# Kernel optimization log

Hardware: AMD Instinct MI355X
Metric: run time of the kernel (lower is better)

Reference implementation:

```python
import jax, jax.numpy as jnp
from jax import lax
import numpy as np

EPS_DENOM = 1e-5
EPS_NCC = 1e-5
HIGH = 0.5  # IntensityNormalization(high=0.5): min-max rescale of weights to [0, high]


def _box_conv(v, kernel):
    # Dense ones-kernel 3D box filter, VALID padding, stride 1 (NCDHW / OIDHW).
    return lax.conv_general_dilated(
        v, kernel, window_strides=(1, 1, 1), padding='VALID',
        dimension_numbers=('NCDHW', 'OIDHW', 'NCDHW'))


def setup_inputs() -> dict:
    key = jax.random.key(0)
    k1, k2 = jax.random.split(key)
    shape = (2, 1, 160, 192, 160)
    y_pred = jax.random.normal(k1, shape, dtype=jnp.float32)
    y_true = jax.random.normal(k2, shape, dtype=jnp.float32)
    kernel = jnp.ones((1, 1, 7, 7, 7), dtype=jnp.float32)
    return {"y_pred": y_pred, "y_true": y_true, "kernel": kernel}


def reference(y_pred, y_true, kernel):
    nw = kernel.sum()  # = 343 for a 7^3 ones kernel
    x, y = y_pred, y_true
    sum_x = _box_conv(x, kernel)
    sum_y = _box_conv(y, kernel)
    sum_x2 = _box_conv(x * x, kernel)
    sum_y2 = _box_conv(y * y, kernel)
    sum_xy = _box_conv(x * y, kernel)

    mean_x = sum_x / nw
    mean_y = sum_y / nw
    num = sum_xy + mean_x * mean_y * nw - mean_x * sum_y - mean_y * sum_x
    denom_0 = mean_x * mean_x * nw + sum_x2 - 2.0 * mean_x * sum_x
    denom_1 = mean_y * mean_y * nw + sum_y2 - 2.0 * mean_y * sum_y
    denom = denom_0 * denom_1

    valid = denom > EPS_DENOM
    safe_denom = jnp.where(valid, denom, 1.0)
    ncc = jnp.where(valid, num / jnp.sqrt(safe_denom), 0.0)
    invalid = (ncc < -1.0 - EPS_NCC) | (ncc > 1.0 + EPS_NCC)
    ncc = jnp.where(invalid, 0.0, ncc)
    all_valid = valid & ~invalid

    # Intensity normalization of weights: min-max rescale of local variance sum
    # over the valid voxels to [0, HIGH], then normalize to sum to 1.
    v = 0.5 * (denom_0 + denom_1)
    vmin = jnp.min(jnp.where(all_valid, v, jnp.inf))
    vmax = jnp.max(jnp.where(all_valid, v, -jnp.inf))
    w = jnp.where(all_valid, (v - vmin) / (vmax - vmin + 1e-12) * HIGH, 0.0)
    w = w / w.sum()

    return 1.0 - jnp.sum(jnp.where(all_valid, ncc, 0.0) * w)
```

## Files before the change

kernel.cpp:

```cpp
#include <hip/hip_runtime.h>
#include <math.h>

#define NN 2
#define DD 160
#define HH 192
#define WW 160
#define DO 154
#define HO 186
#define WO 154

#define NWO 3
#define HOT 8
#define NHO 24
#define ZCH 7
#define ZOC 22
#define NSL 28
#define NB (NWO * NHO * NN * ZCH)

#define LDS_SYNC() do { __builtin_amdgcn_s_waitcnt(0xC07F); __builtin_amdgcn_s_barrier(); } while (0)

__device__ __forceinline__ float block_sum(float v, float* sm) {
  int tid = threadIdx.x;
  sm[tid] = v;
  __syncthreads();
#pragma unroll
  for (int off = 128; off > 0; off >>= 1) {
    if (tid < off) sm[tid] += sm[tid + off];
    __syncthreads();
  }
  float r = sm[0];
  __syncthreads();
  return r;
}

__device__ __forceinline__ float block_min(float v, float* sm) {
  int tid = threadIdx.x;
  sm[tid] = v;
  __syncthreads();
#pragma unroll
  for (int off = 128; off > 0; off >>= 1) {
    if (tid < off) sm[tid] = fminf(sm[tid], sm[tid + off]);
    __syncthreads();
  }
  float r = sm[0];
  __syncthreads();
  return r;
}

__device__ __forceinline__ float wave_sum(float v) {
  v += __shfl_xor(v, 32); v += __shfl_xor(v, 16); v += __shfl_xor(v, 8);
  v += __shfl_xor(v, 4);  v += __shfl_xor(v, 2);  v += __shfl_xor(v, 1);
  return v;
}

__device__ __forceinline__ float wave_min(float v) {
  v = fminf(v, __shfl_xor(v, 32)); v = fminf(v, __shfl_xor(v, 16));
  v = fminf(v, __shfl_xor(v, 8));  v = fminf(v, __shfl_xor(v, 4));
  v = fminf(v, __shfl_xor(v, 2));  v = fminf(v, __shfl_xor(v, 1));
  return v;
}

#define SLIDE7(V, M) do { \
  float s0 = ((V[0]+V[1])+(V[2]+V[3])) + ((V[4]+V[5])+V[6]); \
  float s1 = s0 - V[0] + V[7]; \
  float s2 = s1 - V[1] + V[8]; \
  float s3 = s2 - V[2] + V[9]; \
  *(float4*)&R[M][rA][c4] = make_float4(s0, s1, s2, s3); \
} while (0)

__global__ __launch_bounds__(256, 3) void ncc_fused(const float* __restrict__ X,
                                                    const float* __restrict__ Y,
                                                    float* __restrict__ part) {
  __shared__ __align__(16) float R[5][14][64];
  __shared__ __align__(16) float Mh[5][HOT][64];
  __shared__ float red[4][5];

  const int tid = threadIdx.x;
  const int tx = tid & 63, ty = tid >> 6;
  const int wo0 = blockIdx.x * 64;
  const int ho0 = blockIdx.y * HOT;
  const int n   = blockIdx.z / ZCH;
  const int ck  = blockIdx.z % ZCH;
  const int z0  = ck * ZOC;

  const int wo = wo0 + tx;
  const bool act0 = (wo < WO) && (ho0 + ty < HO);
  const bool act1 = (wo < WO) && (ho0 + ty + 4 < HO);

  const size_t slice = (size_t)HH * WW;
  const float* Xn = X + (size_t)n * DD * slice;
  const float* Yn = Y + (size_t)n * DD * slice;
  const float inv_nw = 1.0f / 343.0f;
  const float LO = -1.0f - 1e-5f, HI = 1.0f + 1e-5f;

  const int pA  = tid;
  const bool hasA = (pA < 224);
  const int rA  = pA >> 4;
  const int c4  = (pA & 15) << 2;
  const int hA  = ho0 + rA;
  const int baseW = wo0 + c4;
  const bool okA  = hasA && (hA < HH) && (baseW < WO);
  const bool tail = okA && (baseW + 10 > WW);
  const float* XrowA = Xn + (size_t)hA * WW + baseW;
  const float* YrowA = Yn + (size_t)hA * WW + baseW;

  float4 lx0={0,0,0,0}, lx1={0,0,0,0};
  float4 ly0={0,0,0,0}, ly1={0,0,0,0};
  float2 lx2={0,0}, ly2={0,0};

  auto loadA = [&](int s_in) {
    if (okA) {
      const float* xp = XrowA + (size_t)(z0 + s_in) * slice;
      const float* yp = YrowA + (size_t)(z0 + s_in) * slice;
      lx0 = *(const float4*)xp;       lx1 = *(const float4*)(xp + 4);
      ly0 = *(const float4*)yp;       ly1 = *(const float4*)(yp + 4);
      if (!tail) { lx2 = *(const float2*)(xp + 8); ly2 = *(const float2*)(yp + 8); }
      else       { lx2 = make_float2(0.f, 0.f);    ly2 = make_float2(0.f, 0.f); }
    }
  };

  auto storeA = [&]() {
    if (okA) {
      const float x[10] = {lx0.x,lx0.y,lx0.z,lx0.w, lx1.x,lx1.y,lx1.z,lx1.w, lx2.x,lx2.y};
      const float y[10] = {ly0.x,ly0.y,ly0.z,ly0.w, ly1.x,ly1.y,ly1.z,ly1.w, ly2.x,ly2.y};
      SLIDE7(x, 0);
      SLIDE7(y, 1);
      {
        float t[10];
#pragma unroll
        for (int i = 0; i < 10; ++i) t[i] = x[i] * x[i];
        SLIDE7(t, 2);
      }
      {
        float t[10];
#pragma unroll
        for (int i = 0; i < 10; ++i) t[i] = y[i] * y[i];
        SLIDE7(t, 3);
      }
      {
        float t[10];
#pragma unroll
        for (int i = 0; i < 10; ++i) t[i] = x[i] * y[i];
        SLIDE7(t, 4);
      }
    }
  };

  auto phaseHitem = [&](int ch, int w) {
    const float* rp = &R[ch][0][w];
    float r0=rp[0],   r1=rp[64],  r2=rp[128], r3=rp[192], r4=rp[256],
          r5=rp[320], r6=rp[384], r7=rp[448], r8=rp[512], r9=rp[576],
          r10=rp[640], r11=rp[704], r12=rp[768], r13=rp[832];
    float m0 = ((r0+r1)+(r2+r3)) + ((r4+r5)+r6);
    float m1 = m0 - r0 + r7;
    float m2 = m1 - r1 + r8;
    float m3 = m2 - r2 + r9;
    float m4 = m3 - r3 + r10;
    float m5 = m4 - r4 + r11;
    float m6 = m5 - r5 + r12;
    float m7 = m6 - r6 + r13;
    Mh[ch][0][w]=m0; Mh[ch][1][w]=m1; Mh[ch][2][w]=m2; Mh[ch][3][w]=m3;
    Mh[ch][4][w]=m4; Mh[ch][5][w]=m5; Mh[ch][6][w]=m6; Mh[ch][7][w]=m7;
  };
  auto phaseH = [&]() {
    phaseHitem(ty, tx);
    if (ty == 3) phaseHitem(4, tx);
  };

  float zs0[2]={0,0}, zs1[2]={0,0}, zs2[2]={0,0}, zs3[2]={0,0}, zs4[2]={0,0};
  float h0[2][7], h1[2][7], h2[2][7], h3[2][7], h4[2][7];
#pragma unroll
  for (int j = 0; j < 7; ++j) {
    h0[0][j]=0.f; h1[0][j]=0.f; h2[0][j]=0.f; h3[0][j]=0.f; h4[0][j]=0.f;
    h0[1][j]=0.f; h1[1][j]=0.f; h2[1][j]=0.f; h3[1][j]=0.f; h4[1][j]=0.f;
  }
  float p_snv = 0.f, p_sn = 0.f, p_sv = 0.f, p_cnt = 0.f, p_vmin = 3.4e38f;

  loadA(0);
  storeA();
  __syncthreads();

#pragma unroll 1
  for (int sb = 0; sb < NSL; sb += 7) {
#pragma unroll
    for (int u = 0; u < 7; ++u) {
      const int s = sb + u;
      if (s + 1 < NSL) loadA(s + 1);
      phaseH();
      LDS_SYNC();
      {
#pragma unroll
        for (int rb = 0; rb < 2; ++rb) {
          const int row = ty + (rb << 2);
          float m0 = Mh[0][row][tx], m1 = Mh[1][row][tx], m2 = Mh[2][row][tx],
                m3 = Mh[3][row][tx], m4 = Mh[4][row][tx];
          zs0[rb] += m0 - h0[rb][u]; h0[rb][u] = m0;
          zs1[rb] += m1 - h1[rb][u]; h1[rb][u] = m1;
          zs2[rb] += m2 - h2[rb][u]; h2[rb][u] = m2;
          zs3[rb] += m3 - h3[rb][u]; h3[rb][u] = m3;
          zs4[rb] += m4 - h4[rb][u]; h4[rb][u] = m4;
          if (s >= 6 && (rb ? act1 : act0)) {
            float num = zs4[rb] - zs0[rb] * zs1[rb] * inv_nw;
            float d0  = zs2[rb] - zs0[rb] * zs0[rb] * inv_nw;
            float d1  = zs3[rb] - zs1[rb] * zs1[rb] * inv_nw;
            float den = d0 * d1;
            if (den > 1e-5f) {
              float ncc = num * __frsqrt_rn(den);
              if (ncc >= LO && ncc <= HI) {
                float v = 0.5f * (d0 + d1);
                p_snv += ncc * v; p_sn += ncc; p_sv += v; p_cnt += 1.f;
                p_vmin = fminf(p_vmin, v);
              }
            }
          }
        }
      }
      if (s + 1 < NSL) storeA();
      LDS_SYNC();
    }
  }

  float r0 = wave_sum(p_snv);
  float r1 = wave_sum(p_sn);
  float r2 = wave_sum(p_sv);
  float r3 = wave_sum(p_cnt);
  float r4 = wave_min(p_vmin);
  if (tx == 0) {
    red[ty][0]=r0; red[ty][1]=r1; red[ty][2]=r2; red[ty][3]=r3; red[ty][4]=r4;
  }
  __syncthreads();
  if (tid == 0) {
    float s0 = (red[0][0]+red[1][0]) + (red[2][0]+red[3][0]);
    float s1 = (red[0][1]+red[1][1]) + (red[2][1]+red[3][1]);
    float s2 = (red[0][2]+red[1][2]) + (red[2][2]+red[3][2]);
    float s3 = (red[0][3]+red[1][3]) + (red[2][3]+red[3][3]);
    float s4 = fminf(fminf(red[0][4],red[1][4]), fminf(red[2][4],red[3][4]));
    const int bid = blockIdx.x + NWO * (blockIdx.y + NHO * blockIdx.z);
    float* pp = part + (size_t)bid * 8;
    pp[0] = s0; pp[1] = s1; pp[2] = s2; pp[3] = s3; pp[4] = s4;
  }
}

__global__ __launch_bounds__(256) void fin(const float* __restrict__ part,
                                           float* __restrict__ out) {
  __shared__ float sm[256];
  const int tid = threadIdx.x;
  float s0 = 0.f, s1 = 0.f, s2 = 0.f, s3 = 0.f, vm = 3.4e38f;
  for (int b = tid; b < NB; b += 256) {
    const float* pp = part + (size_t)b * 8;
    s0 += pp[0]; s1 += pp[1]; s2 += pp[2]; s3 += pp[3];
    vm = fminf(vm, pp[4]);
  }
  s0 = block_sum(s0, sm);
  s1 = block_sum(s1, sm);
  s2 = block_sum(s2, sm);
  s3 = block_sum(s3, sm);
  vm = block_min(vm, sm);
  if (tid == 0) {
    out[0] = 1.0f - (s0 - vm * s1) / (s2 - vm * s3);
  }
}

extern "C" void kernel_launch(void* const* d_in, const int* in_sizes, int n_in,
                              void* d_out, int out_size, void* d_ws, size_t ws_size,
                              hipStream_t stream) {
  const float* X = (const float*)d_in[0];
  const float* Y = (const float*)d_in[1];

  float* part = (float*)d_ws;

  dim3 g(NWO, NHO, NN * ZCH);
  ncc_fused<<<g, 256, 0, stream>>>(X, Y, part);
  fin<<<1, 256, 0, stream>>>(part, (float*)d_out);
}
```

Measured before the change: 159.8 us.

## Prefetch input slices two steps ahead and vectorize H-pass with float2

```diff
diff --git a/kernel.cpp b/kernel.cpp
--- a/kernel.cpp
+++ b/kernel.cpp
@@ -60,12 +60,95 @@
   return v;
 }
 
+__device__ __forceinline__ float2 f2add(float2 a, float2 b) {
+  return make_float2(a.x + b.x, a.y + b.y);
+}
+__device__ __forceinline__ float2 f2slide(float2 m, float2 s, float2 n) {
+  return make_float2(m.x - s.x + n.x, m.y - s.y + n.y);
+}
+
 #define SLIDE7(V, M) do { \
   float s0 = ((V[0]+V[1])+(V[2]+V[3])) + ((V[4]+V[5])+V[6]); \
   float s1 = s0 - V[0] + V[7]; \
   float s2 = s1 - V[1] + V[8]; \
   float s3 = s2 - V[2] + V[9]; \
   *(float4*)&R[M][rA][c4] = make_float4(s0, s1, s2, s3); \
+} while (0)
+
+#define LOADA(P, SIN) do { if (okA) { \
+  const float* xp = XrowA + (size_t)(z0 + (SIN)) * slice; \
+  const float* yp = YrowA + (size_t)(z0 + (SIN)) * slice; \
+  lx0_##P = *(const float4*)xp;       lx1_##P = *(const float4*)(xp + 4); \
+  ly0_##P = *(const float4*)yp;       ly1_##P = *(const float4*)(yp + 4); \
+  if (!tail) { lx2_##P = *(const float2*)(xp + 8); ly2_##P = *(const float2*)(yp + 8); } \
+  else       { lx2_##P = make_float2(0.f, 0.f);    ly2_##P = make_float2(0.f, 0.f); } \
+} } while (0)
+
+#define STOREA(P) do { if (okA) { \
+  const float x[10] = {lx0_##P.x,lx0_##P.y,lx0_##P.z,lx0_##P.w, \
+                       lx1_##P.x,lx1_##P.y,lx1_##P.z,lx1_##P.w, lx2_##P.x,lx2_##P.y}; \
+  const float y[10] = {ly0_##P.x,ly0_##P.y,ly0_##P.z,ly0_##P.w, \
+                       ly1_##P.x,ly1_##P.y,ly1_##P.z,ly1_##P.w, ly2_##P.x,ly2_##P.y}; \
+  SLIDE7(x, 0); \
+  SLIDE7(y, 1); \
+  { float t[10]; \
+    _Pragma("unroll") for (int i = 0; i < 10; ++i) t[i] = x[i] * x[i]; \
+    SLIDE7(t, 2); } \
+  { float t[10]; \
+    _Pragma("unroll") for (int i = 0; i < 10; ++i) t[i] = y[i] * y[i]; \
+    SLIDE7(t, 3); } \
+  { float t[10]; \
+    _Pragma("unroll") for (int i = 0; i < 10; ++i) t[i] = x[i] * y[i]; \
+    SLIDE7(t, 4); } \
+} } while (0)
+
+#define PHASEO(U, S) do { \
+  float ma0 = Mh[0][ty][tx], mb0 = Mh[0][ty+4][tx]; \
+  float ma1 = Mh[1][ty][tx], mb1 = Mh[1][ty+4][tx]; \
+  float ma2 = Mh[2][ty][tx], mb2 = Mh[2][ty+4][tx]; \
+  float ma3 = Mh[3][ty][tx], mb3 = Mh[3][ty+4][tx]; \
+  float ma4 = Mh[4][ty][tx], mb4 = Mh[4][ty+4][tx]; \
+  zs0[0] += ma0 - h0[0][U]; h0[0][U] = ma0;  zs0[1] += mb0 - h0[1][U]; h0[1][U] = mb0; \
+  zs1[0] += ma1 - h1[0][U]; h1[0][U] = ma1;  zs1[1] += mb1 - h1[1][U]; h1[1][U] = mb1; \
+  zs2[0] += ma2 - h2[0][U]; h2[0][U] = ma2;  zs2[1] += mb2 - h2[1][U]; h2[1][U] = mb2; \
+  zs3[0] += ma3 - h3[0][U]; h3[0][U] = ma3;  zs3[1] += mb3 - h3[1][U]; h3[1][U] = mb3; \
+  zs4[0] += ma4 - h4[0][U]; h4[0][U] = ma4;  zs4[1] += mb4 - h4[1][U]; h4[1][U] = mb4; \
+  if ((S) >= 6) { \
+    if (act0) { \
+      float num = zs4[0] - zs0[0] * zs1[0] * inv_nw; \
+      float d0  = zs2[0] - zs0[0] * zs0[0] * inv_nw; \
+      float d1  = zs3[0] - zs1[0] * zs1[0] * inv_nw; \
+      float den = d0 * d1; \
+      if (den > 1e-5f) { \
+        float ncc = num * __frsqrt_rn(den); \
+        if (ncc >= LO && ncc <= HI) { \
+          float v = 0.5f * (d0 + d1); \
+          p_snv += ncc * v; p_sn += ncc; p_sv += v; p_cnt += 1.f; \
+          p_vmin = fminf(p_vmin, v); \
+        } } } \
+    if (act1) { \
+      float num = zs4[1] - zs0[1] * zs1[1] * inv_nw; \
+      float d0  = zs2[1] - zs0[1] * zs0[1] * inv_nw; \
+      float d1  = zs3[1] - zs1[1] * zs1[1] * inv_nw; \
+      float den = d0 * d1; \
+      if (den > 1e-5f) { \
+        float ncc = num * __frsqrt_rn(den); \
+        if (ncc >= LO && ncc <= HI) { \
+          float v = 0.5f * (d0 + d1); \
+          p_snv += ncc * v; p_sn += ncc; p_sv += v; p_cnt += 1.f; \
+          p_vmin = fminf(p_vmin, v); \
+        } } } \
+  } \
+} while (0)
+
+#define STEP(K, P, Q, U) do { \
+  const int s = base + (K); \
+  if (s + 2 < NSL) LOADA(P, s + 2); \
+  phaseH(); \
+  LDS_SYNC(); \
+  PHASEO(U, s); \
+  if (s + 1 < NSL) STOREA(Q); \
+  LDS_SYNC(); \
 } while (0)
 
 __global__ __launch_bounds__(256, 3) void ncc_fused(const float* __restrict__ X,
@@ -104,67 +187,32 @@
   const float* XrowA = Xn + (size_t)hA * WW + baseW;
   const float* YrowA = Yn + (size_t)hA * WW + baseW;
 
-  float4 lx0={0,0,0,0}, lx1={0,0,0,0};
-  float4 ly0={0,0,0,0}, ly1={0,0,0,0};
-  float2 lx2={0,0}, ly2={0,0};
-
-  auto loadA = [&](int s_in) {
-    if (okA) {
-      const float* xp = XrowA + (size_t)(z0 + s_in) * slice;
-      const float* yp = YrowA + (size_t)(z0 + s_in) * slice;
-      lx0 = *(const float4*)xp;       lx1 = *(const float4*)(xp + 4);
-      ly0 = *(const float4*)yp;       ly1 = *(const float4*)(yp + 4);
-      if (!tail) { lx2 = *(const float2*)(xp + 8); ly2 = *(const float2*)(yp + 8); }
-      else       { lx2 = make_float2(0.f, 0.f);    ly2 = make_float2(0.f, 0.f); }
+  float4 lx0_0={0,0,0,0}, lx1_0={0,0,0,0}; float2 lx2_0={0,0};
+  float4 ly0_0={0,0,0,0}, ly1_0={0,0,0,0}; float2 ly2_0={0,0};
+  float4 lx0_1={0,0,0,0}, lx1_1={0,0,0,0}; float2 lx2_1={0,0};
+  float4 ly0_1={0,0,0,0}, ly1_1={0,0,0,0}; float2 ly2_1={0,0};
+
+  const bool okH = (tx < 32) || (ty == 3);
+  const int chH = (tx < 32) ? ty : 4;
+  const int wpH = tx & 31;
+  const float2* rpH = (const float2*)&R[chH][0][0] + wpH;
+  float2* mhH = (float2*)&Mh[chH][0][0] + wpH;
+
+  auto phaseH = [&]() {
+    if (okH) {
+      float2 r0 = rpH[0],   r1 = rpH[32],  r2 = rpH[64],  r3 = rpH[96],
+             r4 = rpH[128], r5 = rpH[160], r6 = rpH[192];
+      float2 m = f2add(f2add(f2add(r0, r1), f2add(r2, r3)), f2add(f2add(r4, r5), r6));
+      mhH[0] = m;
+      float2 nw;
+      nw = rpH[224]; m = f2slide(m, r0, nw); mhH[32]  = m;
+      nw = rpH[256]; m = f2slide(m, r1, nw); mhH[64]  = m;
+      nw = rpH[288]; m = f2slide(m, r2, nw); mhH[96]  = m;
+      nw = rpH[320]; m = f2slide(m, r3, nw); mhH[128] = m;
+      nw = rpH[352]; m = f2slide(m, r4, nw); mhH[160] = m;
+      nw = rpH[384]; m = f2slide(m, r5, nw); mhH[192] = m;
+      nw = rpH[416]; m = f2slide(m, r6, nw); mhH[224] = m;
     }
-  };
-
-  auto storeA = [&]() {
-    if (okA) {
-      const float x[10] = {lx0.x,lx0.y,lx0.z,lx0.w, lx1.x,lx1.y,lx1.z,lx1.w, lx2.x,lx2.y};
-      const float y[10] = {ly0.x,ly0.y,ly0.z,ly0.w, ly1.x,ly1.y,ly1.z,ly1.w, ly2.x,ly2.y};
-      SLIDE7(x, 0);
-      SLIDE7(y, 1);
-      {
-        float t[10];
-#pragma unroll
-        for (int i = 0; i < 10; ++i) t[i] = x[i] * x[i];
-        SLIDE7(t, 2);
-      }
-      {
-        float t[10];
-#pragma unroll
-        for (int i = 0; i < 10; ++i) t[i] = y[i] * y[i];
-        SLIDE7(t, 3);
-      }
-      {
-        float t[10];
-#pragma unroll
-        for (int i = 0; i < 10; ++i) t[i] = x[i] * y[i];
-        SLIDE7(t, 4);
-      }
-    }
-  };
-
-  auto phaseHitem = [&](int ch, int w) {
-    const float* rp = &R[ch][0][w];
-    float r0=rp[0],   r1=rp[64],  r2=rp[128], r3=rp[192], r4=rp[256],
-          r5=rp[320], r6=rp[384], r7=rp[448], r8=rp[512], r9=rp[576],
-          r10=rp[640], r11=rp[704], r12=rp[768], r13=rp[832];
-    float m0 = ((r0+r1)+(r2+r3)) + ((r4+r5)+r6);
-    float m1 = m0 - r0 + r7;
-    float m2 = m1 - r1 + r8;
-    float m3 = m2 - r2 + r9;
-    float m4 = m3 - r3 + r10;
-    float m5 = m4 - r4 + r11;
-    float m6 = m5 - r5 + r12;
-    float m7 = m6 - r6 + r13;
-    Mh[ch][0][w]=m0; Mh[ch][1][w]=m1; Mh[ch][2][w]=m2; Mh[ch][3][w]=m3;
-    Mh[ch][4][w]=m4; Mh[ch][5][w]=m5; Mh[ch][6][w]=m6; Mh[ch][7][w]=m7;
-  };
-  auto phaseH = [&]() {
-    phaseHitem(ty, tx);
-    if (ty == 3) phaseHitem(4, tx);
   };
 
   float zs0[2]={0,0}, zs1[2]={0,0}, zs2[2]={0,0}, zs3[2]={0,0}, zs4[2]={0,0};
@@ -176,48 +224,27 @@
   }
   float p_snv = 0.f, p_sn = 0.f, p_sv = 0.f, p_cnt = 0.f, p_vmin = 3.4e38f;
 
-  loadA(0);
-  storeA();
+  LOADA(0, 0);
+  LOADA(1, 1);
+  STOREA(0);
   __syncthreads();
 
 #pragma unroll 1
-  for (int sb = 0; sb < NSL; sb += 7) {
-#pragma unroll
-    for (int u = 0; u < 7; ++u) {
-      const int s = sb + u;
-      if (s + 1 < NSL) loadA(s + 1);
-      phaseH();
-      LDS_SYNC();
-      {
-#pragma unroll
-        for (int rb = 0; rb < 2; ++rb) {
-          const int row = ty + (rb << 2);
-          float m0 = Mh[0][row][tx], m1 = Mh[1][row][tx], m2 = Mh[2][row][tx],
-                m3 = Mh[3][row][tx], m4 = Mh[4][row][tx];
-          zs0[rb] += m0 - h0[rb][u]; h0[rb][u] = m0;
-          zs1[rb] += m1 - h1[rb][u]; h1[rb][u] = m1;
-          zs2[rb] += m2 - h2[rb][u]; h2[rb][u] = m2;
-          zs3[rb] += m3 - h3[rb][u]; h3[rb][u] = m3;
-          zs4[rb] += m4 - h4[rb][u]; h4[rb][u] = m4;
-          if (s >= 6 && (rb ? act1 : act0)) {
-            float num = zs4[rb] - zs0[rb] * zs1[rb] * inv_nw;
-            float d0  = zs2[rb] - zs0[rb] * zs0[rb] * inv_nw;
-            float d1  = zs3[rb] - zs1[rb] * zs1[rb] * inv_nw;
-            float den = d0 * d1;
-            if (den > 1e-5f) {
-              float ncc = num * __frsqrt_rn(den);
-              if (ncc >= LO && ncc <= HI) {
-                float v = 0.5f * (d0 + d1);
-                p_snv += ncc * v; p_sn += ncc; p_sv += v; p_cnt += 1.f;
-                p_vmin = fminf(p_vmin, v);
-              }
-            }
-          }
-        }
-      }
-      if (s + 1 < NSL) storeA();
-      LDS_SYNC();
-    }
+  for (int base = 0; base < NSL; base += 14) {
+    STEP(0, 0, 1, 0);
+    STEP(1, 1, 0, 1);
+    STEP(2, 0, 1, 2);
+    STEP(3, 1, 0, 3);
+    STEP(4, 0, 1, 4);
+    STEP(5, 1, 0, 5);
+    STEP(6, 0, 1, 6);
+    STEP(7, 1, 0, 0);
+    STEP(8, 0, 1, 1);
+    STEP(9, 1, 0, 2);
+    STEP(10, 0, 1, 3);
+    STEP(11, 1, 0, 4);
+    STEP(12, 0, 1, 5);
+    STEP(13, 1, 0, 6);
   }
 
   float r0 = wave_sum(p_snv);
```

Measured after the change: 232.5 us. +45.5%, slower.
